# Performance work log

Hardware: AMD Instinct MI355X
Metric: run time of the kernel (lower is better)

## Reference

```python
import jax, jax.numpy as jnp
import numpy as np

N_NODES = 50000
N_EDGES = 800000
IN_DIM = 128
EDGE_DIM = 32
HID = 64


def _glorot(key, shape):
    fan_in, fan_out = shape[0], shape[1]
    lim = float(np.sqrt(6.0 / (fan_in + fan_out)))
    return jax.random.uniform(key, shape, jnp.float32, -lim, lim)


def setup_inputs() -> dict:
    key = jax.random.key(0)
    ks = jax.random.split(key, 16)
    x = jax.random.normal(ks[0], (N_NODES, IN_DIM), jnp.float32)
    edge_index = jax.random.randint(ks[1], (2, N_EDGES), 0, N_NODES, jnp.int64)
    edge_attr = jax.random.normal(ks[2], (N_EDGES, EDGE_DIM), jnp.float32)
    message = jax.random.normal(ks[3], (N_EDGES, HID), jnp.float32)
    return {
        "x": x,
        "edge_index": edge_index,
        "edge_attr": edge_attr,
        "message": message,
        "W_src": _glorot(ks[4], (IN_DIM, HID)),
        "W_dest": _glorot(ks[5], (IN_DIM, HID)),
        "W_edge": _glorot(ks[6], (EDGE_DIM, HID)),
        "attn_vec": _glorot(ks[7], (1, HID)),
        "mlp_w1": _glorot(ks[8], (2 * HID, HID)),
        "mlp_b1": jnp.zeros((HID,), jnp.float32),
        "bn1_g": jnp.ones((HID,), jnp.float32),
        "bn1_b": jnp.zeros((HID,), jnp.float32),
        "mlp_w2": _glorot(ks[9], (HID, HID)),
        "mlp_b2": jnp.zeros((HID,), jnp.float32),
        "bn2_g": jnp.ones((HID,), jnp.float32),
        "bn2_b": jnp.zeros((HID,), jnp.float32),
        "amlp_w": _glorot(ks[10], (HID, 1)),
        "amlp_b": jnp.zeros((1,), jnp.float32),
    }


def _batchnorm(h, g, b, eps=1e-5):
    mu = jnp.mean(h, axis=0)
    var = jnp.var(h, axis=0)  # biased, as torch BN training forward
    return (h - mu) * jax.lax.rsqrt(var + eps) * g + b


def _segment_softmax(scores, seg, num_segments):
    m = jax.ops.segment_max(scores, seg, num_segments=num_segments)
    m = jnp.where(jnp.isneginf(m), 0.0, m)
    e = jnp.exp(scores - m[seg])
    s = jax.ops.segment_sum(e, seg, num_segments=num_segments)
    return e / s[seg]


def _scatter_max0(vals, seg, num_segments):
    # torch_scatter reduce='max' fills empty segments with 0
    out = jax.ops.segment_max(vals, seg, num_segments=num_segments)
    return jnp.where(jnp.isneginf(out), 0.0, out)


def reference(x, edge_index, edge_attr, message, W_src, W_dest, W_edge, attn_vec,
              mlp_w1, mlp_b1, bn1_g, bn1_b, mlp_w2, mlp_b2, bn2_g, bn2_b,
              amlp_w, amlp_b):
    row, col = edge_index[0], edge_index[1]
    # attention scores per edge
    h = x[row] @ W_src + x[col] @ W_dest + edge_attr @ W_edge  # [E, H]
    scores = jax.nn.leaky_relu(h @ attn_vec[0], negative_slope=0.2)  # [E]
    attn = _segment_softmax(scores, col, N_NODES)  # [E]
    msg = message * attn[:, None]  # [E, H]
    fwd = _scatter_max0(msg, col, N_NODES)  # [N, H]
    bwd = _scatter_max0(msg, row, N_NODES)  # [N, H]
    out = jnp.concatenate([fwd, bwd], axis=1)  # [N, 2H]
    # node MLP (BatchNorm in training-stats mode, dropout disabled)
    h1 = jax.nn.relu(_batchnorm(out @ mlp_w1 + mlp_b1, bn1_g, bn1_b))
    h2 = jax.nn.relu(_batchnorm(h1 @ mlp_w2 + mlp_b2, bn2_g, bn2_b))
    gate = jax.nn.sigmoid(h2 @ amlp_w + amlp_b).reshape(-1)  # [N]
    return h2, gate
```

## Files before the change

kernel.cpp:

```cpp
#include <hip/hip_runtime.h>
#include <hip/hip_bf16.h>
#include <float.h>

#define IN_DIM 128
#define EDGE_DIM 32
#define HID 64
#define BKT_G 64
#define BCAP 3072
#define NBKT_MAX 784
#define CHUNK 4096

__global__ void k_uvw(const float* __restrict__ Wsrc, const float* __restrict__ Wdst,
                      const float* __restrict__ Wedge, const float* __restrict__ avec,
                      const int* __restrict__ ei32, int* sflag,
                      float* u, float* v, float* w,
                      int* gcur, float* stats, int nbkt) {
    int gt = blockIdx.x * blockDim.x + threadIdx.x;
    int gstride = gridDim.x * blockDim.x;
    for (int i = gt; i < 2 * nbkt; i += gstride) gcur[i] = 0;
    for (int i = gt; i < 512; i += gstride) stats[i] = 0.0f;
    if (gt == 0) {
        int odd_or = ei32[1] | ei32[3] | ei32[5] | ei32[7] | ei32[9] | ei32[11];
        sflag[0] = (odd_or == 0) ? 2 : 1;
    }
    int wave = gt >> 6;
    int lane = threadIdx.x & 63;
    const float* src; float* dst; int row;
    if (wave < 128)      { src = Wsrc;  dst = u; row = wave; }
    else if (wave < 256) { src = Wdst;  dst = v; row = wave - 128; }
    else if (wave < 288) { src = Wedge; dst = w; row = wave - 256; }
    else return;
    float acc = src[row * HID + lane] * avec[lane];
    for (int o = 32; o >= 1; o >>= 1) acc += __shfl_xor(acc, o);
    if (lane == 0) dst[row] = acc;
}

__global__ void k_pq(const float* __restrict__ x, const float* __restrict__ u,
                     const float* __restrict__ v, float* p, float* q, int N) {
    int wave = (blockIdx.x * blockDim.x + threadIdx.x) >> 6;
    int lane = threadIdx.x & 63;
    if (wave >= N) return;
    const float* xr = x + (size_t)wave * IN_DIM;
    float a0 = xr[lane], a1 = xr[lane + 64];
    float pp = a0 * u[lane] + a1 * u[lane + 64];
    float qq = a0 * v[lane] + a1 * v[lane + 64];
    for (int m = 32; m >= 1; m >>= 1) { pp += __shfl_xor(pp, m); qq += __shfl_xor(qq, m); }
    if (lane == 0) { p[wave] = pp; q[wave] = qq; }
}

__global__ void k_edot(const float* __restrict__ ea, const float* __restrict__ w,
                       float* rdot, int E) {
    int gid = blockIdx.x * blockDim.x + threadIdx.x;
    int e = gid >> 3;
    int j = gid & 7;
    if (e >= E) return;
    float4 av = ((const float4*)ea)[(size_t)e * 8 + j];
    float4 wv = ((const float4*)w)[j];
    float val = av.x * wv.x + av.y * wv.y + av.z * wv.z + av.w * wv.w;
    val += __shfl_xor(val, 4);
    val += __shfl_xor(val, 2);
    val += __shfl_xor(val, 1);
    if (j == 0) rdot[e] = val;
}

__global__ __launch_bounds__(256) void k_binscore(const int* __restrict__ ei,
                                                  const int* __restrict__ sflag,
                                                  const float* __restrict__ rdot,
                                                  const float* __restrict__ p,
                                                  const float* __restrict__ q,
                                                  float* scores,
                                                  int* gcur_col, int* gcur_row,
                                                  unsigned* bbuf_col, unsigned* bbuf_row,
                                                  int E, int nbkt) {
    __shared__ int lc[NBKT_MAX], lrw[NBKT_MAX];
    __shared__ int gc[NBKT_MAX], grw[NBKT_MAX];
    int tid = threadIdx.x;
    int e0 = blockIdx.x * CHUNK;
    int e1 = e0 + CHUNK; if (e1 > E) e1 = E;
    for (int i = tid; i < nbkt; i += 256) { lc[i] = 0; lrw[i] = 0; }
    __syncthreads();
    int st = sflag[0];
    for (int e = e0 + tid; e < e1; e += 256) {
        int r = ei[(size_t)st * e];
        int c = ei[(size_t)st * (E + e)];
        float sc = rdot[e] + p[r] + q[c];
        scores[e] = (sc > 0.f) ? sc : 0.2f * sc;
        atomicAdd(&lc[c >> 6], 1);
        atomicAdd(&lrw[r >> 6], 1);
    }
    __syncthreads();
    for (int b = tid; b < nbkt; b += 256) {
        int n1 = lc[b];  if (n1) gc[b]  = atomicAdd(&gcur_col[b], n1);
        int n2 = lrw[b]; if (n2) grw[b] = atomicAdd(&gcur_row[b], n2);
        lc[b] = 0; lrw[b] = 0;
    }
    __syncthreads();
    for (int e = e0 + tid; e < e1; e += 256) {
        int r = ei[(size_t)st * e];
        int c = ei[(size_t)st * (E + e)];
        int pos = gc[c >> 6] + atomicAdd(&lc[c >> 6], 1);
        if (pos < BCAP) bbuf_col[(size_t)(c >> 6) * BCAP + pos] = (unsigned)((e << 6) | (c & 63));
        int pos2 = grw[r >> 6] + atomicAdd(&lrw[r >> 6], 1);
        if (pos2 < BCAP) bbuf_row[(size_t)(r >> 6) * BCAP + pos2] = (unsigned)((e << 6) | (r & 63));
    }
}

__global__ __launch_bounds__(512) void k_sortfwd(float* scores, const float* __restrict__ msg,
                                                 const int* __restrict__ bcur,
                                                 const unsigned* __restrict__ bbuf,
                                                 float* fwd, int N) {
    __shared__ unsigned raw[BCAP];
    __shared__ unsigned srt[BCAP];
    __shared__ float    ssc[BCAP];
    __shared__ int cnt[BKT_G], cur[BKT_G], sstart[BKT_G + 1];
    int b = blockIdx.x, tid = threadIdx.x;
    int M = bcur[b]; if (M > BCAP) M = BCAP;
    if (tid < BKT_G) cnt[tid] = 0;
    __syncthreads();
    for (int i = tid; i < M; i += 512) {
        unsigned v = bbuf[(size_t)b * BCAP + i];
        raw[i] = v;
        atomicAdd(&cnt[v & 63], 1);
    }
    __syncthreads();
    if (tid < BKT_G) {
        int val = cnt[tid];
        int inc = val;
        for (int off = 1; off < BKT_G; off <<= 1) {
            int o = __shfl_up(inc, off);
            if (tid >= off) inc += o;
        }
        sstart[tid + 1] = inc;
        if (tid == 0) sstart[0] = 0;
        cur[tid] = inc - val;
    }
    __syncthreads();
    for (int j = tid; j < M; j += 512) {
        unsigned v = raw[j];
        int posn = atomicAdd(&cur[v & 63], 1);
        srt[posn] = v;
    }
    __syncthreads();
    for (int i = tid; i < M; i += 512) ssc[i] = scores[srt[i] >> 6];
    __syncthreads();
    int wave = tid >> 6, lane = tid & 63;
    for (int n = wave; n < BKT_G; n += 8) {
        int node = b * BKT_G + n;
        if (node >= N) continue;
        int a0 = sstart[n], len = sstart[n + 1] - a0;
        if (len == 0) { fwd[(size_t)node * HID + lane] = 0.f; continue; }
        float m = -FLT_MAX;
        for (int k = lane; k < len; k += 64) m = fmaxf(m, ssc[a0 + k]);
        for (int o = 32; o >= 1; o >>= 1) m = fmaxf(m, __shfl_xor(m, o));
        float ssum = 0.f;
        for (int k = lane; k < len; k += 64) ssum += expf(ssc[a0 + k] - m);
        for (int o = 32; o >= 1; o >>= 1) ssum += __shfl_xor(ssum, o);
        float rcp = 1.f / ssum;
        for (int k = lane; k < len; k += 64) {
            int i = a0 + k;
            float at = expf(ssc[i] - m) * rcp;
            ssc[i] = at;
            scores[srt[i] >> 6] = at;
        }
        asm volatile("s_waitcnt lgkmcnt(0)" ::: "memory");
        float acc = -FLT_MAX;
        int k = 0;
        for (; k + 8 <= len; k += 8) {
            float vv[8];
#pragma unroll
            for (int u8 = 0; u8 < 8; u8++) {
                int i = a0 + k + u8;
                vv[u8] = msg[(size_t)(srt[i] >> 6) * HID + lane] * ssc[i];
            }
#pragma unroll
            for (int u8 = 0; u8 < 8; u8++) acc = fmaxf(acc, vv[u8]);
        }
        for (; k < len; k++) {
            int i = a0 + k;
            acc = fmaxf(acc, msg[(size_t)(srt[i] >> 6) * HID + lane] * ssc[i]);
        }
        fwd[(size_t)node * HID + lane] = acc;
    }
}

__global__ __launch_bounds__(512) void k_sortbwd(const float* __restrict__ scores,
                                                 const float* __restrict__ msg,
                                                 const int* __restrict__ bcur,
                                                 const unsigned* __restrict__ bbuf,
                                                 float* bwd, int N) {
    __shared__ unsigned raw[BCAP];
    __shared__ unsigned srt[BCAP];
    __shared__ float    ssc[BCAP];
    __shared__ int cnt[BKT_G], cur[BKT_G], sstart[BKT_G + 1];
    int b = blockIdx.x, tid = threadIdx.x;
    int M = bcur[b]; if (M > BCAP) M = BCAP;
    if (tid < BKT_G) cnt[tid] = 0;
    __syncthreads();
    for (int i = tid; i < M; i += 512) {
        unsigned v = bbuf[(size_t)b * BCAP + i];
        raw[i] = v;
        atomicAdd(&cnt[v & 63], 1);
    }
    __syncthreads();
    if (tid < BKT_G) {
        int val = cnt[tid];
        int inc = val;
        for (int off = 1; off < BKT_G; off <<= 1) {
            int o = __shfl_up(inc, off);
            if (tid >= off) inc += o;
        }
        sstart[tid + 1] = inc;
        if (tid == 0) sstart[0] = 0;
        cur[tid] = inc - val;
    }
    __syncthreads();
    for (int j = tid; j < M; j += 512) {
        unsigned v = raw[j];
        int posn = atomicAdd(&cur[v & 63], 1);
        srt[posn] = v;
    }
    __syncthreads();
    for (int i = tid; i < M; i += 512) ssc[i] = scores[srt[i] >> 6];
    __syncthreads();
    int wave = tid >> 6, lane = tid & 63;
    for (int n = wave; n < BKT_G; n += 8) {
        int node = b * BKT_G + n;
        if (node >= N) continue;
        int a0 = sstart[n], len = sstart[n + 1] - a0;
        if (len == 0) { bwd[(size_t)node * HID + lane] = 0.f; continue; }
        float acc = -FLT_MAX;
        int k = 0;
        for (; k + 8 <= len; k += 8) {
            float vv[8];
#pragma unroll
            for (int u8 = 0; u8 < 8; u8++) {
                int i = a0 + k + u8;
                vv[u8] = msg[(size_t)(srt[i] >> 6) * HID + lane] * ssc[i];
            }
#pragma unroll
            for (int u8 = 0; u8 < 8; u8++) acc = fmaxf(acc, vv[u8]);
        }
        for (; k < len; k++) {
            int i = a0 + k;
            acc = fmaxf(acc, msg[(size_t)(srt[i] >> 6) * HID + lane] * ssc[i]);
        }
        bwd[(size_t)node * HID + lane] = acc;
    }
}

__global__ __launch_bounds__(256) void k_mlp1(const float* __restrict__ fwd,
                                              const float* __restrict__ bwd,
                                              const float* __restrict__ W1,
                                              const float* __restrict__ b1,
                                              float* pre1, float* gsum, float* gss, int N) {
    __shared__ float lsum[HID], lss[HID];
    int t = threadIdx.x;
    if (t < HID) { lsum[t] = 0.f; lss[t] = 0.f; }
    __syncthreads();
    int h = t & 63, lr = t >> 6;
    float bh = b1[h];
    float s = 0.f, ssq = 0.f;
    for (int n = blockIdx.x * 4 + lr; n < N; n += gridDim.x * 4) {
        const float* fr = fwd + (size_t)n * HID;
        const float* br = bwd + (size_t)n * HID;
        float acc = bh;
        for (int k = 0; k < HID; k++) acc += fr[k] * W1[k * HID + h];
        for (int k = 0; k < HID; k++) acc += br[k] * W1[(HID + k) * HID + h];
        pre1[(size_t)n * HID + h] = acc;
        s += acc; ssq += acc * acc;
    }
    atomicAdd(&lsum[h], s);
    atomicAdd(&lss[h], ssq);
    __syncthreads();
    if (t < HID) { atomicAdd(&gsum[t], lsum[t]); atomicAdd(&gss[t], lss[t]); }
}

__global__ void k_bnfin(const float* __restrict__ gsum, const float* __restrict__ gss,
                        const float* __restrict__ g, const float* __restrict__ b,
                        float* scale, float* shift, int N) {
    int t = threadIdx.x;
    if (t >= HID) return;
    float invN = 1.0f / (float)N;
    float mu = gsum[t] * invN;
    float var = gss[t] * invN - mu * mu;
    float rs = rsqrtf(var + 1e-5f);
    float sc = rs * g[t];
    scale[t] = sc;
    shift[t] = b[t] - mu * sc;
}

__global__ __launch_bounds__(256) void k_mlp2(const float* __restrict__ pre1,
                                              const float* __restrict__ scale1,
                                              const float* __restrict__ shift1,
                                              const float* __restrict__ W2,
                                              const float* __restrict__ b2v,
                                              float* pre2, float* gsum, float* gss, int N) {
    __shared__ float lsum[HID], lss[HID];
    int t = threadIdx.x;
    if (t < HID) { lsum[t] = 0.f; lss[t] = 0.f; }
    __syncthreads();
    int h = t & 63, lr = t >> 6;
    float bh = b2v[h];
    float s = 0.f, ssq = 0.f;
    for (int n = blockIdx.x * 4 + lr; n < N; n += gridDim.x * 4) {
        const float* pr = pre1 + (size_t)n * HID;
        float acc = bh;
        for (int k = 0; k < HID; k++) {
            float z = pr[k] * scale1[k] + shift1[k];
            z = (z > 0.f) ? z : 0.f;
            acc += z * W2[k * HID + h];
        }
        pre2[(size_t)n * HID + h] = acc;
        s += acc; ssq += acc * acc;
    }
    atomicAdd(&lsum[h], s);
    atomicAdd(&lss[h], ssq);
    __syncthreads();
    if (t < HID) { atomicAdd(&gsum[t], lsum[t]); atomicAdd(&gss[t], lss[t]); }
}

__global__ void k_out(const float* __restrict__ pre2, const float* __restrict__ scale2,
                      const float* __restrict__ shift2, const float* __restrict__ amw,
                      const float* __restrict__ amb, float* out, int N) {
    int gid = blockIdx.x * blockDim.x + threadIdx.x;
    int n = gid >> 6, h = gid & 63;
    if (n >= N) return;
    float z = pre2[(size_t)n * HID + h] * scale2[h] + shift2[h];
    float h2 = (z > 0.f) ? z : 0.f;
    out[(size_t)n * HID + h] = h2;
    float part = h2 * amw[h];
    for (int m = 32; m >= 1; m >>= 1) part += __shfl_xor(part, m);
    if (h == 0) {
        float gate = 1.0f / (1.0f + expf(-(part + amb[0])));
        out[(size_t)N * HID + n] = gate;
    }
}

extern "C" void kernel_launch(void* const* d_in, const int* in_sizes, int n_in,
                              void* d_out, int out_size, void* d_ws, size_t ws_size,
                              hipStream_t stream) {
    const float* x     = (const float*)d_in[0];
    const int*   ei    = (const int*)d_in[1];
    const float* ea    = (const float*)d_in[2];
    const float* msg   = (const float*)d_in[3];
    const float* Wsrc  = (const float*)d_in[4];
    const float* Wdst  = (const float*)d_in[5];
    const float* Wedge = (const float*)d_in[6];
    const float* avec  = (const float*)d_in[7];
    const float* W1    = (const float*)d_in[8];
    const float* b1    = (const float*)d_in[9];
    const float* g1    = (const float*)d_in[10];
    const float* bb1   = (const float*)d_in[11];
    const float* W2    = (const float*)d_in[12];
    const float* b2    = (const float*)d_in[13];
    const float* g2    = (const float*)d_in[14];
    const float* bb2   = (const float*)d_in[15];
    const float* amw   = (const float*)d_in[16];
    const float* amb   = (const float*)d_in[17];
    float* out = (float*)d_out;

    const int N = in_sizes[0] / IN_DIM;
    const int E = in_sizes[1] / 2;
    const int NH = N * HID;
    const int nbkt = (N + BKT_G - 1) / BKT_G;

    float* ws = (float*)d_ws;
    float* gsum1  = ws;
    float* gss1   = ws + 64;
    float* gsum2  = ws + 128;
    float* gss2   = ws + 192;
    float* scale1 = ws + 256;
    float* shift1 = ws + 320;
    float* scale2 = ws + 384;
    float* shift2 = ws + 448;
    int*   sflag  = (int*)(ws + 512);
    float* u      = ws + 576;
    float* v      = ws + 704;
    float* w      = ws + 832;
    float* T        = ws + 1024;
    float* p        = T;
    float* q        = p + N;
    float* scores   = q + N;
    float* rdot     = scores + E;
    int*   gcur_col = (int*)(rdot + E);
    int*   gcur_row = gcur_col + nbkt;
    unsigned* bbuf_col = (unsigned*)(gcur_row + nbkt);
    unsigned* bbuf_row = bbuf_col + (size_t)nbkt * BCAP;
    size_t T_words  = 2 * (size_t)N + 2 * (size_t)E + 2 * (size_t)nbkt
                    + 2 * (size_t)nbkt * BCAP;
    size_t T_sz     = (T_words < (size_t)NH) ? (size_t)NH : T_words;
    float* fwd  = ws + 1024 + T_sz;
    float* bwd  = fwd + (size_t)NH;
    float* pre1 = T;
    float* pre2 = fwd;

    hipLaunchKernelGGL(k_uvw, dim3(72), dim3(256), 0, stream,
                       Wsrc, Wdst, Wedge, avec, ei, sflag, u, v, w,
                       gcur_col, ws, nbkt);
    hipLaunchKernelGGL(k_pq, dim3((N * 64 + 255) / 256), dim3(256), 0, stream,
                       x, u, v, p, q, N);
    hipLaunchKernelGGL(k_edot, dim3((E * 8 + 255) / 256), dim3(256), 0, stream,
                       ea, w, rdot, E);
    hipLaunchKernelGGL(k_binscore, dim3((E + CHUNK - 1) / CHUNK), dim3(256), 0, stream,
                       ei, sflag, rdot, p, q, scores,
                       gcur_col, gcur_row, bbuf_col, bbuf_row, E, nbkt);
    hipLaunchKernelGGL(k_sortfwd, dim3(nbkt), dim3(512), 0, stream,
                       scores, msg, gcur_col, bbuf_col, fwd, N);
    hipLaunchKernelGGL(k_sortbwd, dim3(nbkt), dim3(512), 0, stream,
                       scores, msg, gcur_row, bbuf_row, bwd, N);
    hipLaunchKernelGGL(k_mlp1, dim3(1024), dim3(256), 0, stream,
                       fwd, bwd, W1, b1, pre1, gsum1, gss1, N);
    hipLaunchKernelGGL(k_bnfin, dim3(1), dim3(64), 0, stream,
                       gsum1, gss1, g1, bb1, scale1, shift1, N);
    hipLaunchKernelGGL(k_mlp2, dim3(1024), dim3(256), 0, stream,
                       pre1, scale1, shift1, W2, b2, pre2, gsum2, gss2, N);
    hipLaunchKernelGGL(k_bnfin, dim3(1), dim3(64), 0, stream,
                       gsum2, gss2, g2, bb2, scale2, shift2, N);
    hipLaunchKernelGGL(k_out, dim3((N * 64 + 255) / 256), dim3(256), 0, stream,
                       pre2, scale2, shift2, amw, amb, out, N);
}
```

Measured before the change: 367.5 us.

## Merge small kernels, dynamic node scheduling, and deeper unroll in scatter-max

Combines the per-node and per-edge dot-product kernels into one launch and folds the two batchnorm-finalize kernels into the consuming MLP and output kernels. This removes three launches and their serialization gaps. The sort/scatter kernels now hand out nodes to waves through a shared atomic counter instead of a fixed stride, which balances uneven degrees. A 16-wide unrolled gather loop adds more memory-level parallelism. The trade-offs are extra register pressure and redundant BN-finalize work done in every block.

After: 376.9 us. 2.6% more time.

```diff
diff --git a/kernel.cpp b/kernel.cpp
--- a/kernel.cpp
+++ b/kernel.cpp
@@ -35,32 +35,33 @@
     if (lane == 0) dst[row] = acc;
 }
 
-__global__ void k_pq(const float* __restrict__ x, const float* __restrict__ u,
-                     const float* __restrict__ v, float* p, float* q, int N) {
-    int wave = (blockIdx.x * blockDim.x + threadIdx.x) >> 6;
-    int lane = threadIdx.x & 63;
-    if (wave >= N) return;
-    const float* xr = x + (size_t)wave * IN_DIM;
-    float a0 = xr[lane], a1 = xr[lane + 64];
-    float pp = a0 * u[lane] + a1 * u[lane + 64];
-    float qq = a0 * v[lane] + a1 * v[lane + 64];
-    for (int m = 32; m >= 1; m >>= 1) { pp += __shfl_xor(pp, m); qq += __shfl_xor(qq, m); }
-    if (lane == 0) { p[wave] = pp; q[wave] = qq; }
-}
-
-__global__ void k_edot(const float* __restrict__ ea, const float* __restrict__ w,
-                       float* rdot, int E) {
-    int gid = blockIdx.x * blockDim.x + threadIdx.x;
-    int e = gid >> 3;
-    int j = gid & 7;
-    if (e >= E) return;
-    float4 av = ((const float4*)ea)[(size_t)e * 8 + j];
-    float4 wv = ((const float4*)w)[j];
-    float val = av.x * wv.x + av.y * wv.y + av.z * wv.z + av.w * wv.w;
-    val += __shfl_xor(val, 4);
-    val += __shfl_xor(val, 2);
-    val += __shfl_xor(val, 1);
-    if (j == 0) rdot[e] = val;
+__global__ void k_pqdot(const float* __restrict__ x, const float* __restrict__ u,
+                        const float* __restrict__ v,
+                        const float* __restrict__ ea, const float* __restrict__ w,
+                        float* p, float* q, float* rdot, int N, int E, int pqBlocks) {
+    if ((int)blockIdx.x < pqBlocks) {
+        int wave = (blockIdx.x * blockDim.x + threadIdx.x) >> 6;
+        int lane = threadIdx.x & 63;
+        if (wave >= N) return;
+        const float* xr = x + (size_t)wave * IN_DIM;
+        float a0 = xr[lane], a1 = xr[lane + 64];
+        float pp = a0 * u[lane] + a1 * u[lane + 64];
+        float qq = a0 * v[lane] + a1 * v[lane + 64];
+        for (int m = 32; m >= 1; m >>= 1) { pp += __shfl_xor(pp, m); qq += __shfl_xor(qq, m); }
+        if (lane == 0) { p[wave] = pp; q[wave] = qq; }
+    } else {
+        int gid = (blockIdx.x - pqBlocks) * blockDim.x + threadIdx.x;
+        int e = gid >> 3;
+        int j = gid & 7;
+        if (e >= E) return;
+        float4 av = ((const float4*)ea)[(size_t)e * 8 + j];
+        float4 wv = ((const float4*)w)[j];
+        float val = av.x * wv.x + av.y * wv.y + av.z * wv.z + av.w * wv.w;
+        val += __shfl_xor(val, 4);
+        val += __shfl_xor(val, 2);
+        val += __shfl_xor(val, 1);
+        if (j == 0) rdot[e] = val;
+    }
 }
 
 __global__ __launch_bounds__(256) void k_binscore(const int* __restrict__ ei,
@@ -113,9 +114,11 @@
     __shared__ unsigned srt[BCAP];
     __shared__ float    ssc[BCAP];
     __shared__ int cnt[BKT_G], cur[BKT_G], sstart[BKT_G + 1];
+    __shared__ int nodectr;
     int b = blockIdx.x, tid = threadIdx.x;
     int M = bcur[b]; if (M > BCAP) M = BCAP;
     if (tid < BKT_G) cnt[tid] = 0;
+    if (tid == 0) nodectr = 0;
     __syncthreads();
     for (int i = tid; i < M; i += 512) {
         unsigned v = bbuf[(size_t)b * BCAP + i];
@@ -143,11 +146,15 @@
     __syncthreads();
     for (int i = tid; i < M; i += 512) ssc[i] = scores[srt[i] >> 6];
     __syncthreads();
-    int wave = tid >> 6, lane = tid & 63;
-    for (int n = wave; n < BKT_G; n += 8) {
-        int node = b * BKT_G + n;
+    int lane = tid & 63;
+    while (true) {
+        int n0;
+        if (lane == 0) n0 = atomicAdd(&nodectr, 1);
+        n0 = __shfl(n0, 0);
+        if (n0 >= BKT_G) break;
+        int node = b * BKT_G + n0;
         if (node >= N) continue;
-        int a0 = sstart[n], len = sstart[n + 1] - a0;
+        int a0 = sstart[n0], len = sstart[n0 + 1] - a0;
         if (len == 0) { fwd[(size_t)node * HID + lane] = 0.f; continue; }
         float m = -FLT_MAX;
         for (int k = lane; k < len; k += 64) m = fmaxf(m, ssc[a0 + k]);
@@ -165,6 +172,16 @@
         asm volatile("s_waitcnt lgkmcnt(0)" ::: "memory");
         float acc = -FLT_MAX;
         int k = 0;
+        for (; k + 16 <= len; k += 16) {
+            float vv[16];
+#pragma unroll
+            for (int u16 = 0; u16 < 16; u16++) {
+                int i = a0 + k + u16;
+                vv[u16] = msg[(size_t)(srt[i] >> 6) * HID + lane] * ssc[i];
+            }
+#pragma unroll
+            for (int u16 = 0; u16 < 16; u16++) acc = fmaxf(acc, vv[u16]);
+        }
         for (; k + 8 <= len; k += 8) {
             float vv[8];
 #pragma unroll
@@ -192,9 +209,11 @@
     __shared__ unsigned srt[BCAP];
     __shared__ float    ssc[BCAP];
     __shared__ int cnt[BKT_G], cur[BKT_G], sstart[BKT_G + 1];
+    __shared__ int nodectr;
     int b = blockIdx.x, tid = threadIdx.x;
     int M = bcur[b]; if (M > BCAP) M = BCAP;
     if (tid < BKT_G) cnt[tid] = 0;
+    if (tid == 0) nodectr = 0;
     __syncthreads();
     for (int i = tid; i < M; i += 512) {
         unsigned v = bbuf[(size_t)b * BCAP + i];
@@ -222,14 +241,28 @@
     __syncthreads();
     for (int i = tid; i < M; i += 512) ssc[i] = scores[srt[i] >> 6];
     __syncthreads();
-    int wave = tid >> 6, lane = tid & 63;
-    for (int n = wave; n < BKT_G; n += 8) {
-        int node = b * BKT_G + n;
+    int lane = tid & 63;
+    while (true) {
+        int n0;
+        if (lane == 0) n0 = atomicAdd(&nodectr, 1);
+        n0 = __shfl(n0, 0);
+        if (n0 >= BKT_G) break;
+        int node = b * BKT_G + n0;
         if (node >= N) continue;
-        int a0 = sstart[n], len = sstart[n + 1] - a0;
+        int a0 = sstart[n0], len = sstart[n0 + 1] - a0;
         if (len == 0) { bwd[(size_t)node * HID + lane] = 0.f; continue; }
         float acc = -FLT_MAX;
         int k = 0;
+        for (; k + 16 <= len; k += 16) {
+            float vv[16];
+#pragma unroll
+            for (int u16 = 0; u16 < 16; u16++) {
+                int i = a0 + k + u16;
+                vv[u16] = msg[(size_t)(srt[i] >> 6) * HID + lane] * ssc[i];
+            }
+#pragma unroll
+            for (int u16 = 0; u16 < 16; u16++) acc = fmaxf(acc, vv[u16]);
+        }
         for (; k + 8 <= len; k += 8) {
             float vv[8];
 #pragma unroll
@@ -275,29 +308,27 @@
     if (t < HID) { atomicAdd(&gsum[t], lsum[t]); atomicAdd(&gss[t], lss[t]); }
 }
 
-__global__ void k_bnfin(const float* __restrict__ gsum, const float* __restrict__ gss,
-                        const float* __restrict__ g, const float* __restrict__ b,
-                        float* scale, float* shift, int N) {
-    int t = threadIdx.x;
-    if (t >= HID) return;
-    float invN = 1.0f / (float)N;
-    float mu = gsum[t] * invN;
-    float var = gss[t] * invN - mu * mu;
-    float rs = rsqrtf(var + 1e-5f);
-    float sc = rs * g[t];
-    scale[t] = sc;
-    shift[t] = b[t] - mu * sc;
-}
-
 __global__ __launch_bounds__(256) void k_mlp2(const float* __restrict__ pre1,
-                                              const float* __restrict__ scale1,
-                                              const float* __restrict__ shift1,
+                                              const float* __restrict__ gsum1,
+                                              const float* __restrict__ gss1,
+                                              const float* __restrict__ g1,
+                                              const float* __restrict__ bb1,
                                               const float* __restrict__ W2,
                                               const float* __restrict__ b2v,
                                               float* pre2, float* gsum, float* gss, int N) {
     __shared__ float lsum[HID], lss[HID];
+    __shared__ float sc1[HID], sh1[HID];
     int t = threadIdx.x;
-    if (t < HID) { lsum[t] = 0.f; lss[t] = 0.f; }
+    if (t < HID) {
+        lsum[t] = 0.f; lss[t] = 0.f;
+        float invN = 1.0f / (float)N;
+        float mu = gsum1[t] * invN;
+        float var = gss1[t] * invN - mu * mu;
+        float rs = rsqrtf(var + 1e-5f);
+        float s1 = rs * g1[t];
+        sc1[t] = s1;
+        sh1[t] = bb1[t] - mu * s1;
+    }
     __syncthreads();
     int h = t & 63, lr = t >> 6;
     float bh = b2v[h];
@@ -306,7 +337,7 @@
         const float* pr = pre1 + (size_t)n * HID;
         float acc = bh;
         for (int k = 0; k < HID; k++) {
-            float z = pr[k] * scale1[k] + shift1[k];
+            float z = pr[k] * sc1[k] + sh1[k];
             z = (z > 0.f) ? z : 0.f;
             acc += z * W2[k * HID + h];
         }
@@ -319,13 +350,30 @@
     if (t < HID) { atomicAdd(&gsum[t], lsum[t]); atomicAdd(&gss[t], lss[t]); }
 }
 
-__global__ void k_out(const float* __restrict__ pre2, const float* __restrict__ scale2,
-                      const float* __restrict__ shift2, const float* __restrict__ amw,
-                      const float* __restrict__ amb, float* out, int N) {
-    int gid = blockIdx.x * blockDim.x + threadIdx.x;
+__global__ __launch_bounds__(256) void k_out(const float* __restrict__ pre2,
+                                             const float* __restrict__ gsum2,
+                                             const float* __restrict__ gss2,
+                                             const float* __restrict__ g2,
+                                             const float* __restrict__ bb2,
+                                             const float* __restrict__ amw,
+                                             const float* __restrict__ amb,
+                                             float* out, int N) {
+    __shared__ float sc2[HID], sh2[HID];
+    int t = threadIdx.x;
+    if (t < HID) {
+        float invN = 1.0f / (float)N;
+        float mu = gsum2[t] * invN;
+        float var = gss2[t] * invN - mu * mu;
+        float rs = rsqrtf(var + 1e-5f);
+        float s2 = rs * g2[t];
+        sc2[t] = s2;
+        sh2[t] = bb2[t] - mu * s2;
+    }
+    __syncthreads();
+    int gid = blockIdx.x * blockDim.x + t;
     int n = gid >> 6, h = gid & 63;
     if (n >= N) return;
-    float z = pre2[(size_t)n * HID + h] * scale2[h] + shift2[h];
+    float z = pre2[(size_t)n * HID + h] * sc2[h] + sh2[h];
     float h2 = (z > 0.f) ? z : 0.f;
     out[(size_t)n * HID + h] = h2;
     float part = h2 * amw[h];
@@ -369,10 +417,6 @@
     float* gss1   = ws + 64;
     float* gsum2  = ws + 128;
     float* gss2   = ws + 192;
-    float* scale1 = ws + 256;
-    float* shift1 = ws + 320;
-    float* scale2 = ws + 384;
-    float* shift2 = ws + 448;
     int*   sflag  = (int*)(ws + 512);
     float* u      = ws + 576;
     float* v      = ws + 704;
@@ -394,13 +438,14 @@
     float* pre1 = T;
     float* pre2 = fwd;
 
+    const int pqBlocks   = (N * 64 + 255) / 256;
+    const int edotBlocks = (E * 8 + 255) / 256;
+
     hipLaunchKernelGGL(k_uvw, dim3(72), dim3(256), 0, stream,
                        Wsrc, Wdst, Wedge, avec, ei, sflag, u, v, w,
                        gcur_col, ws, nbkt);
-    hipLaunchKernelGGL(k_pq, dim3((N * 64 + 255) / 256), dim3(256), 0, stream,
-                       x, u, v, p, q, N);
-    hipLaunchKernelGGL(k_edot, dim3((E * 8 + 255) / 256), dim3(256), 0, stream,
-                       ea, w, rdot, E);
+    hipLaunchKernelGGL(k_pqdot, dim3(pqBlocks + edotBlocks), dim3(256), 0, stream,
+                       x, u, v, ea, w, p, q, rdot, N, E, pqBlocks);
     hipLaunchKernelGGL(k_binscore, dim3((E + CHUNK - 1) / CHUNK), dim3(256), 0, stream,
                        ei, sflag, rdot, p, q, scores,
                        gcur_col, gcur_row, bbuf_col, bbuf_row, E, nbkt);
@@ -410,12 +455,8 @@
                        scores, msg, gcur_row, bbuf_row, bwd, N);
     hipLaunchKernelGGL(k_mlp1, dim3(1024), dim3(256), 0, stream,
                        fwd, bwd, W1, b1, pre1, gsum1, gss1, N);
-    hipLaunchKernelGGL(k_bnfin, dim3(1), dim3(64), 0, stream,
-                       gsum1, gss1, g1, bb1, scale1, shift1, N);
     hipLaunchKernelGGL(k_mlp2, dim3(1024), dim3(256), 0, stream,
-                       pre1, scale1, shift1, W2, b2, pre2, gsum2, gss2, N);
-    hipLaunchKernelGGL(k_bnfin, dim3(1), dim3(64), 0, stream,
-                       gsum2, gss2, g2, bb2, scale2, shift2, N);
-    hipLaunchKernelGGL(k_out, dim3((N * 64 + 255) / 256), dim3(256), 0, stream,
-                       pre2, scale2, shift2, amw, amb, out, N);
-}
+                       pre1, gsum1, gss1, g1, bb1, W2, b2, pre2, gsum2, gss2, N);
+    hipLaunchKernelGGL(k_out, dim3(pqBlocks), dim3(256), 0, stream,
+                       pre2, gsum2, gss2, g2, bb2, amw, amb, out, N);
+}
```
